# Kernel optimization log

Hardware: AMD Instinct MI355X
Metric: run time of the kernel (lower is better)

The kernel has to match this reference:

```python
import jax, jax.numpy as jnp
import numpy as np

Q_DIM = 2048
HEADS = 16
HEAD_DIM = 128
INNER = HEADS * HEAD_DIM          # 2048
MLP_HID = int(Q_DIM * 4.0)        # 8192
MLP_MULT = 2
EPS = 1e-05
B, S = 2, 2048


def setup_inputs() -> dict:
    key = jax.random.key(0)
    ks = jax.random.split(key, 4)
    hidden_states = jax.random.normal(ks[0], (B, S, Q_DIM), dtype=jnp.float32)
    # interleaved RoPE tables: cos/sin of shape [S, HEAD_DIM]
    half = HEAD_DIM // 2
    freqs = 1.0 / (10000.0 ** (np.arange(half, dtype=np.float64) / half))
    ang = np.outer(np.arange(S, dtype=np.float64), freqs)      # [S, half]
    ang = np.repeat(ang, 2, axis=-1)                            # [S, HEAD_DIM]
    rope_cos = jnp.asarray(np.cos(ang), dtype=jnp.float32)
    rope_sin = jnp.asarray(np.sin(ang), dtype=jnp.float32)
    fused_out = 3 * INNER + MLP_HID * MLP_MULT                  # 22528
    W_qkv_mlp = jax.random.normal(ks[1], (Q_DIM, fused_out), dtype=jnp.float32) * (Q_DIM ** -0.5)
    norm_q_w = jnp.ones((HEAD_DIM,), dtype=jnp.float32)
    norm_k_w = jnp.ones((HEAD_DIM,), dtype=jnp.float32)
    W_out = jax.random.normal(ks[2], (INNER + MLP_HID, Q_DIM), dtype=jnp.float32) * ((INNER + MLP_HID) ** -0.5)
    b_out = jnp.zeros((Q_DIM,), dtype=jnp.float32)
    return {"hidden_states": hidden_states, "rope_cos": rope_cos, "rope_sin": rope_sin,
            "W_qkv_mlp": W_qkv_mlp, "norm_q_w": norm_q_w, "norm_k_w": norm_k_w,
            "W_out": W_out, "b_out": b_out}


def _rms_norm(x, w):
    # RMSNorm over the last (head_dim) axis
    return x * jax.lax.rsqrt(jnp.mean(x * x, axis=-1, keepdims=True) + EPS) * w


def _apply_rope(x, cos, sin):
    # x: [B, S, H, D]; interleaved rotate-half (diffusers real-rope convention)
    xr = x.reshape(*x.shape[:-1], HEAD_DIM // 2, 2)
    rot = jnp.stack([-xr[..., 1], xr[..., 0]], axis=-1).reshape(x.shape)
    return x * cos[None, :, None, :] + rot * sin[None, :, None, :]


def reference(hidden_states, rope_cos, rope_sin, W_qkv_mlp, norm_q_w, norm_k_w, W_out, b_out):
    b, s, _ = hidden_states.shape
    proj = hidden_states @ W_qkv_mlp                              # [B,S,22528]
    qkv, mlp_h = jnp.split(proj, [3 * INNER], axis=-1)
    q, k, v = jnp.split(qkv, 3, axis=-1)
    q = q.reshape(b, s, HEADS, HEAD_DIM)
    k = k.reshape(b, s, HEADS, HEAD_DIM)
    v = v.reshape(b, s, HEADS, HEAD_DIM)
    q = _rms_norm(q, norm_q_w)
    k = _rms_norm(k, norm_k_w)
    q = _apply_rope(q, rope_cos, rope_sin)
    k = _apply_rope(k, rope_cos, rope_sin)
    scale = HEAD_DIM ** -0.5
    scores = jnp.einsum('bqhd,bkhd->bhqk', q, k) * scale          # [B,H,S,S]
    attn = jax.nn.softmax(scores, axis=-1)
    out_attn = jnp.einsum('bhqk,bkhd->bqhd', attn, v).reshape(b, s, INNER)
    m1, m2 = jnp.split(mlp_h, 2, axis=-1)                         # SwiGLU
    mlp_out = jax.nn.silu(m1) * m2                                # [B,S,MLP_HID]
    cat = jnp.concatenate([out_attn, mlp_out], axis=-1)           # [B,S,INNER+MLP_HID]
    return cat @ W_out + b_out
```

## Files before the change

### kernel.cpp

```cpp
#include <hip/hip_runtime.h>

typedef unsigned short u16;
typedef unsigned int u32;
typedef __bf16 bf16x8 __attribute__((ext_vector_type(8)));
typedef float f32x4 __attribute__((ext_vector_type(4)));

#define MFMA16(a, b, c) __builtin_amdgcn_mfma_f32_16x16x32_bf16((a), (b), (c), 0, 0, 0)

#define S_LEN 2048
#define D_HEAD 128
#define NHEADS 16
#define NBH 32
#define QDIM 2048
#define NPROJ 22528
#define NQKV 6144
#define NMLP 16384
#define NCAT 10240
#define MROWS 4096

#define BARRIER() __builtin_amdgcn_s_barrier()
#define WAITVM0() asm volatile("s_waitcnt vmcnt(0)" ::: "memory")

__device__ __forceinline__ float bf2f(u16 u) { return __uint_as_float(((u32)u) << 16); }
__device__ __forceinline__ u16 f2bf(float f) {
  u32 u = __float_as_uint(f);
  return (u16)((u + 0x7FFFu + ((u >> 16) & 1u)) >> 16);
}
__device__ __forceinline__ void gld16(const void* g, void* l) {
  __builtin_amdgcn_global_load_lds((__attribute__((address_space(1))) void*)(g),
                                   (__attribute__((address_space(3))) void*)(l), 16, 0, 0);
}

__global__ __launch_bounds__(256) void f32_to_bf16(const float* __restrict__ in,
                                                   u16* __restrict__ out) {
  const u32 i = blockIdx.x * 256 + threadIdx.x;
  const float4 v = ((const float4*)in)[i];
  uint2 o;
  o.x = (u32)f2bf(v.x) | ((u32)f2bf(v.y) << 16);
  o.y = (u32)f2bf(v.z) | ((u32)f2bf(v.w) << 16);
  ((uint2*)out)[i] = o;
}

template <int REMAP>
__global__ __launch_bounds__(256) void transpose_f32_bf16(const float* __restrict__ in,
                                                          u16* __restrict__ out, int R, int C) {
  __shared__ u16 tile[64][65];
  const int tx = threadIdx.x & 63;
  const int ty = threadIdx.x >> 6;
  const int c0 = blockIdx.x * 64;
  const int r0 = blockIdx.y * 64;
#pragma unroll
  for (int it = 0; it < 16; ++it) {
    const int rr = ty * 16 + it;
    tile[rr][tx] = f2bf(in[(size_t)(r0 + rr) * C + c0 + tx]);
  }
  __syncthreads();
#pragma unroll
  for (int it = 0; it < 16; ++it) {
    const int rr = ty * 16 + it;
    int orow = c0 + rr;
    if (REMAP && orow >= NQKV) {
      const int c = orow - NQKV;
      const int f = c & 8191;
      const int sel = c >> 13;
      orow = NQKV + (((f >> 4) << 5) | (sel << 4) | (f & 15));
    }
    out[(size_t)orow * R + r0 + tx] = tile[tx][rr];
  }
}

__global__ __launch_bounds__(256) void transpose_bf16_b(const u16* __restrict__ in,
                                                        u16* __restrict__ out, int R, int C) {
  __shared__ u16 tile[64][65];
  const int z = blockIdx.z;
  in += (size_t)z * R * C;
  out += (size_t)z * R * C;
  const int tx = threadIdx.x & 63;
  const int ty = threadIdx.x >> 6;
  const int c0 = blockIdx.x * 64;
  const int r0 = blockIdx.y * 64;
#pragma unroll
  for (int it = 0; it < 16; ++it) {
    const int rr = ty * 16 + it;
    tile[rr][tx] = in[(size_t)(r0 + rr) * C + c0 + tx];
  }
  __syncthreads();
#pragma unroll
  for (int it = 0; it < 16; ++it) {
    const int rr = ty * 16 + it;
    out[(size_t)(c0 + rr) * R + r0 + tx] = tile[tx][rr];
  }
}

template <int OUTMODE>
__global__ __launch_bounds__(256, 2) void gemm_bt(const u16* __restrict__ A,
                                                  const u16* __restrict__ Bt,
                                                  void* __restrict__ Cvoid,
                                                  const float* __restrict__ bias, int N, int K) {
  __shared__ u16 As[128 * 64];
  __shared__ u16 Bs[128 * 64];
  const int t = threadIdx.x;
  const int l = t & 63;
  const int w = t >> 6;
  const int lr = l & 15;
  const int lg = l >> 4;
  const int m0 = blockIdx.y * 128;
  const int n0 = blockIdx.x * 128;
  const int wm = (w >> 1) * 64;
  const int wn = (w & 1) * 64;

  f32x4 acc[4][4] = {};
  const int obase = w * 1024 + l * 16;

  for (int k0 = 0; k0 < K; k0 += 64) {
#pragma unroll
    for (int rnd = 0; rnd < 4; ++rnd) {
      const int o = obase + rnd * 4096;
      const int row = o >> 7;
      const int g = (o & 127) >> 4;
      const int gs = g ^ (row & 7);
      gld16(A + (size_t)(m0 + row) * K + k0 + gs * 8, &As[rnd * 2048 + w * 512]);
      gld16(Bt + (size_t)(n0 + row) * K + k0 + gs * 8, &Bs[rnd * 2048 + w * 512]);
    }
    __syncthreads();

    bf16x8 af[4][2], bfr[4][2];
#pragma unroll
    for (int i = 0; i < 4; ++i) {
#pragma unroll
      for (int kc = 0; kc < 2; ++kc) {
        const int ra = wm + i * 16 + lr;
        af[i][kc] = *(const bf16x8*)&As[ra * 64 + (((kc * 4 + lg) ^ (ra & 7)) * 8)];
        const int rb = wn + i * 16 + lr;
        bfr[i][kc] = *(const bf16x8*)&Bs[rb * 64 + (((kc * 4 + lg) ^ (rb & 7)) * 8)];
      }
    }
#pragma unroll
    for (int kc = 0; kc < 2; ++kc)
#pragma unroll
      for (int i = 0; i < 4; ++i)
#pragma unroll
        for (int j = 0; j < 4; ++j)
          acc[i][j] = MFMA16(af[i][kc], bfr[j][kc], acc[i][j]);
    __syncthreads();
  }

  if (OUTMODE == 1) {
    float* C = (float*)Cvoid;
#pragma unroll
    for (int i = 0; i < 4; ++i)
#pragma unroll
      for (int j = 0; j < 4; ++j)
#pragma unroll
        for (int r = 0; r < 4; ++r) {
          const int row = m0 + wm + i * 16 + lg * 4 + r;
          const int col = n0 + wn + j * 16 + lr;
          C[(size_t)row * N + col] = acc[i][j][r] + bias[col];
        }
  } else {
    u16* C = (u16*)Cvoid;
#pragma unroll
    for (int i = 0; i < 4; ++i)
#pragma unroll
      for (int jj = 0; jj < 2; ++jj)
#pragma unroll
        for (int r = 0; r < 4; ++r) {
          const int row = m0 + wm + i * 16 + lg * 4 + r;
          const float a1 = acc[i][2 * jj][r];
          const float a2 = acc[i][2 * jj + 1][r];
          const float fz = a1 / (1.f + __expf(-a1)) * a2;
          const int col = ((n0 + wn) >> 1) + jj * 16 + lr;
          C[(size_t)row * N + col] = f2bf(fz);
        }
  }
}

__global__ __launch_bounds__(256, 2) void gemm_qkv(const u16* __restrict__ A,
                                                   const u16* __restrict__ Bt,
                                                   const float* __restrict__ cosT,
                                                   const float* __restrict__ sinT,
                                                   const float* __restrict__ wq,
                                                   const float* __restrict__ wk,
                                                   u16* __restrict__ Qb, u16* __restrict__ Kb,
                                                   u16* __restrict__ Vb, int K) {
  __shared__ u16 As[128 * 64];
  __shared__ u16 Bs[128 * 64];
  __shared__ float redbuf[2][128];
  const int t = threadIdx.x;
  const int l = t & 63;
  const int w = t >> 6;
  const int lr = l & 15;
  const int lg = l >> 4;
  const int m0 = blockIdx.y * 128;
  const int n0 = blockIdx.x * 128;
  const int wm = (w >> 1) * 64;
  const int wn = (w & 1) * 64;

  f32x4 acc[4][4] = {};
  const int obase = w * 1024 + l * 16;

  for (int k0 = 0; k0 < K; k0 += 64) {
#pragma unroll
    for (int rnd = 0; rnd < 4; ++rnd) {
      const int o = obase + rnd * 4096;
      const int row = o >> 7;
      const int g = (o & 127) >> 4;
      const int gs = g ^ (row & 7);
      gld16(A + (size_t)(m0 + row) * K + k0 + gs * 8, &As[rnd * 2048 + w * 512]);
      gld16(Bt + (size_t)(n0 + row) * K + k0 + gs * 8, &Bs[rnd * 2048 + w * 512]);
    }
    __syncthreads();

    bf16x8 af[4][2], bfr[4][2];
#pragma unroll
    for (int i = 0; i < 4; ++i) {
#pragma unroll
      for (int kc = 0; kc < 2; ++kc) {
        const int ra = wm + i * 16 + lr;
        af[i][kc] = *(const bf16x8*)&As[ra * 64 + (((kc * 4 + lg) ^ (ra & 7)) * 8)];
        const int rb = wn + i * 16 + lr;
        bfr[i][kc] = *(const bf16x8*)&Bs[rb * 64 + (((kc * 4 + lg) ^ (rb & 7)) * 8)];
      }
    }
#pragma unroll
    for (int kc = 0; kc < 2; ++kc)
#pragma unroll
      for (int i = 0; i < 4; ++i)
#pragma unroll
        for (int j = 0; j < 4; ++j)
          acc[i][j] = MFMA16(af[i][kc], bfr[j][kc], acc[i][j]);
    __syncthreads();
  }

  const int type = n0 >> 11;
  const int h = (n0 >> 7) & 15;
  u16* dst = (type == 0) ? Qb : (type == 1) ? Kb : Vb;

  if (type == 2) {
#pragma unroll
    for (int i = 0; i < 4; ++i)
#pragma unroll
      for (int j = 0; j < 4; ++j)
#pragma unroll
        for (int r = 0; r < 4; ++r) {
          const int row = m0 + wm + i * 16 + lg * 4 + r;
          const int s = row & 2047, b = row >> 11;
          const int col = wn + j * 16 + lr;
          dst[((size_t)(b * 16 + h) * S_LEN + s) * 128 + col] = f2bf(acc[i][j][r]);
        }
    return;
  }

  float ssum[4][4];
#pragma unroll
  for (int i = 0; i < 4; ++i)
#pragma unroll
    for (int r = 0; r < 4; ++r) {
      float p = acc[i][0][r] * acc[i][0][r] + acc[i][1][r] * acc[i][1][r] +
                acc[i][2][r] * acc[i][2][r] + acc[i][3][r] * acc[i][3][r];
      p += __shfl_xor(p, 1);
      p += __shfl_xor(p, 2);
      p += __shfl_xor(p, 4);
      p += __shfl_xor(p, 8);
      ssum[i][r] = p;
    }
  if (lr == 0) {
#pragma unroll
    for (int i = 0; i < 4; ++i)
#pragma unroll
      for (int r = 0; r < 4; ++r) redbuf[wn >> 6][wm + i * 16 + lg * 4 + r] = ssum[i][r];
  }
  __syncthreads();

  const float* wgt = type ? wk : wq;
  const float sc = type ? 1.0f : 0.12751744f;
#pragma unroll
  for (int i = 0; i < 4; ++i)
#pragma unroll
    for (int r = 0; r < 4; ++r) {
      const int lrow = wm + i * 16 + lg * 4 + r;
      const float tot = redbuf[0][lrow] + redbuf[1][lrow];
      const float rsq = rsqrtf(tot * (1.0f / 128.0f) + 1e-5f) * sc;
      const int row = m0 + lrow;
      const int s = row & 2047, b = row >> 11;
      const size_t rbase = ((size_t)(b * 16 + h) * S_LEN + s) * 128;
#pragma unroll
      for (int j = 0; j < 4; ++j) {
        const int col = wn + j * 16 + lr;
        const float xn = acc[i][j][r] * rsq * wgt[col];
        const float pr = __shfl_xor(xn, 1);
        const float c = cosT[s * 128 + col];
        const float sn = sinT[s * 128 + col];
        const float val = (col & 1) ? (xn * c + pr * sn) : (xn * c - pr * sn);
        dst[rbase + col] = f2bf(val);
      }
    }
}

__global__ __launch_bounds__(256, 2) void attn_fwd(const u16* __restrict__ Qb,
                                                   const u16* __restrict__ Kb,
                                                   const u16* __restrict__ Vt,
                                                   u16* __restrict__ Cat) {
  __shared__ u16 Ks[2][64 * 128];
  __shared__ u16 Vs[2][128 * 64];
  __shared__ u16 Ps[4][32 * 64];

  const int t = threadIdx.x;
  const int l = t & 63;
  const int w = t >> 6;
  const int lr = l & 15;
  const int lg = l >> 4;
  const int swz = (blockIdx.x & 7) * 64 + (blockIdx.x >> 3);
  const int qt = swz & 15;
  const int bh = swz >> 4;
  const int b = bh >> 4;
  const int h = bh & 15;
  const int q0 = qt * 128 + w * 32;
  const int obase = w * 1024 + l * 16;

  const size_t kbase = (size_t)bh * S_LEN * 128;
  const size_t vbase = (size_t)bh * 128 * S_LEN;

  bf16x8 qf[2][4];
#pragma unroll
  for (int im = 0; im < 2; ++im)
#pragma unroll
    for (int kc = 0; kc < 4; ++kc)
      qf[im][kc] =
          *(const bf16x8*)&Qb[((size_t)bh * S_LEN + q0 + im * 16 + lr) * 128 + kc * 32 + lg * 8];

  f32x4 oacc[2][8] = {};
  float lrun[2][4] = {};

  u16* P = Ps[w];

  auto stageKV = [&](int buf, int kt2) {
    const int kk0 = kt2 * 64;
#pragma unroll
    for (int rnd = 0; rnd < 4; ++rnd) {
      const int o = obase + rnd * 4096;
      {
        const int key = o >> 8;
        const int g = (o & 255) >> 4;
        const int gs = g ^ (key & 7);
        gld16(Kb + kbase + (size_t)(kk0 + key) * 128 + gs * 8,
              &Ks[buf][rnd * 2048 + w * 512]);
      }
      {
        const int d = o >> 7;
        const int g = (o & 127) >> 4;
        const int gs = g ^ (d & 7);
        gld16(Vt + vbase + (size_t)d * S_LEN + kk0 + gs * 8,
              &Vs[buf][rnd * 2048 + w * 512]);
      }
    }
  };

  stageKV(0, 0);
  WAITVM0();
  BARRIER();

  int cur = 0;
  for (int kt = 0; kt < 32; ++kt) {
    if (kt + 1 < 32) stageKV(cur ^ 1, kt + 1);

    const u16* Kc = &Ks[cur][0];
    const u16* Vc = &Vs[cur][0];

    f32x4 sf[2][4] = {};
    __builtin_amdgcn_s_setprio(1);
#pragma unroll
    for (int j = 0; j < 4; ++j) {
      const int kr = j * 16 + lr;
      bf16x8 kf[4];
#pragma unroll
      for (int kc = 0; kc < 4; ++kc)
        kf[kc] = *(const bf16x8*)&Kc[kr * 128 + (((kc * 4 + lg) ^ (kr & 7)) * 8)];
#pragma unroll
      for (int kc = 0; kc < 4; ++kc)
#pragma unroll
        for (int im = 0; im < 2; ++im)
          sf[im][j] = MFMA16(qf[im][kc], kf[kc], sf[im][j]);
    }
    __builtin_amdgcn_s_setprio(0);

#pragma unroll
    for (int im = 0; im < 2; ++im)
#pragma unroll
      for (int r = 0; r < 4; ++r) {
        float psum = 0.f;
#pragma unroll
        for (int j = 0; j < 4; ++j) {
          const float pv = exp2f(sf[im][j][r]);
          sf[im][j][r] = pv;
          psum += pv;
        }
        lrun[im][r] += psum;
      }

#pragma unroll
    for (int im = 0; im < 2; ++im)
#pragma unroll
      for (int j = 0; j < 4; ++j)
#pragma unroll
        for (int r = 0; r < 4; ++r) {
          const int q = im * 16 + lg * 4 + r;
          const int key = j * 16 + lr;
          const int g = key >> 3;
          P[q * 64 + ((g ^ (q & 7)) * 8) + (key & 7)] = f2bf(sf[im][j][r]);
        }

    __builtin_amdgcn_s_setprio(1);
#pragma unroll
    for (int kc = 0; kc < 2; ++kc) {
      bf16x8 pa[2];
#pragma unroll
      for (int im = 0; im < 2; ++im) {
        const int q = im * 16 + lr;
        pa[im] = *(const bf16x8*)&P[q * 64 + (((kc * 4 + lg) ^ (q & 7)) * 8)];
      }
#pragma unroll
      for (int df = 0; df < 8; ++df) {
        const int d = df * 16 + lr;
        const bf16x8 vb = *(const bf16x8*)&Vc[d * 64 + (((kc * 4 + lg) ^ (d & 7)) * 8)];
#pragma unroll
        for (int im = 0; im < 2; ++im) oacc[im][df] = MFMA16(pa[im], vb, oacc[im][df]);
      }
    }
    __builtin_amdgcn_s_setprio(0);

    WAITVM0();
    BARRIER();
    cur ^= 1;
  }

#pragma unroll
  for (int im = 0; im < 2; ++im)
#pragma unroll
    for (int r = 0; r < 4; ++r) {
      float tot = lrun[im][r];
      tot += __shfl_xor(tot, 1);
      tot += __shfl_xor(tot, 2);
      tot += __shfl_xor(tot, 4);
      tot += __shfl_xor(tot, 8);
      const float inv = 1.0f / tot;
      const int row = b * S_LEN + q0 + im * 16 + lg * 4 + r;
#pragma unroll
      for (int df = 0; df < 8; ++df) {
        const int col = h * 128 + df * 16 + lr;
        Cat[(size_t)row * NCAT + col] = f2bf(oacc[im][df][r] * inv);
      }
    }
}

extern "C" void kernel_launch(void* const* d_in, const int* in_sizes, int n_in, void* d_out,
                              int out_size, void* d_ws, size_t ws_size, hipStream_t stream) {
  (void)in_sizes; (void)n_in; (void)out_size; (void)ws_size;
  const float* hs = (const float*)d_in[0];
  const float* rcos = (const float*)d_in[1];
  const float* rsin = (const float*)d_in[2];
  const float* Wqkv = (const float*)d_in[3];
  const float* wq = (const float*)d_in[4];
  const float* wk = (const float*)d_in[5];
  const float* Wout = (const float*)d_in[6];
  const float* bout = (const float*)d_in[7];
  float* out = (float*)d_out;

  char* ws = (char*)d_ws;
  size_t off = 0;
  auto nxt = [&](size_t bytes) {
    char* p = ws + off;
    off += (bytes + 255) & ~(size_t)255;
    return p;
  };
  u16* Xb = (u16*)nxt((size_t)MROWS * QDIM * 2);
  u16* Wqkvt = (u16*)nxt((size_t)NPROJ * QDIM * 2);
  u16* Woutt = (u16*)nxt((size_t)QDIM * NCAT * 2);
  u16* Qb = (u16*)nxt((size_t)NBH * S_LEN * D_HEAD * 2);
  u16* Kb = (u16*)nxt((size_t)NBH * S_LEN * D_HEAD * 2);
  u16* Vb = (u16*)nxt((size_t)NBH * S_LEN * D_HEAD * 2);
  u16* Vt = (u16*)nxt((size_t)NBH * S_LEN * D_HEAD * 2);
  u16* Cat = (u16*)nxt((size_t)MROWS * NCAT * 2);

  f32_to_bf16<<<(MROWS * QDIM / 4) / 256, 256, 0, stream>>>(hs, Xb);
  transpose_f32_bf16<1><<<dim3(NPROJ / 64, QDIM / 64), 256, 0, stream>>>(Wqkv, Wqkvt, QDIM,
                                                                         NPROJ);
  transpose_f32_bf16<0><<<dim3(QDIM / 64, NCAT / 64), 256, 0, stream>>>(Wout, Woutt, NCAT, QDIM);

  gemm_qkv<<<dim3(NQKV / 128, MROWS / 128), 256, 0, stream>>>(Xb, Wqkvt, rcos, rsin, wq, wk,
                                                              Qb, Kb, Vb, QDIM);
  gemm_bt<2><<<dim3(NMLP / 128, MROWS / 128), 256, 0, stream>>>(
      Xb, Wqkvt + (size_t)NQKV * QDIM, Cat + QDIM, nullptr, NCAT, QDIM);

  transpose_bf16_b<<<dim3(D_HEAD / 64, S_LEN / 64, NBH), 256, 0, stream>>>(Vb, Vt, S_LEN, D_HEAD);

  attn_fwd<<<S_LEN / 128 * NBH, 256, 0, stream>>>(Qb, Kb, Vt, Cat);

  gemm_bt<1><<<dim3(QDIM / 128, MROWS / 128), 256, 0, stream>>>(Cat, Woutt, out, bout, QDIM,
                                                                NCAT);
}
```

Measured before the change: 772.9 us.

## Fuse V transpose into QKV GEMM epilogue and widen weight transpose tiles

The QKV GEMM now writes V directly in transposed [bh][d][s] layout by staging the tile through swizzled shared memory, which removes the separate V transpose kernel and its intermediate buffer. The fp32-to-bf16 weight transpose now processes 64x256 tiles and writes 8-byte vectorized stores instead of scalar 2-byte stores, to improve write coalescing. The larger shared tile (64x260 u16) lowers occupancy for the transpose kernels, and the V epilogue adds an extra barrier and shared-memory round trip.

Measured after the change: 769.1 us. No clear change (-0.5%).

```diff
diff --git a/kernel.cpp b/kernel.cpp
--- a/kernel.cpp
+++ b/kernel.cpp
@@ -44,51 +44,37 @@
 template <int REMAP>
 __global__ __launch_bounds__(256) void transpose_f32_bf16(const float* __restrict__ in,
                                                           u16* __restrict__ out, int R, int C) {
-  __shared__ u16 tile[64][65];
-  const int tx = threadIdx.x & 63;
-  const int ty = threadIdx.x >> 6;
+  __shared__ u16 tile[64][260];
+  const int t = threadIdx.x;
+  const int tx = t & 63;
+  const int ty = t >> 6;
   const int c0 = blockIdx.x * 64;
-  const int r0 = blockIdx.y * 64;
-#pragma unroll
-  for (int it = 0; it < 16; ++it) {
-    const int rr = ty * 16 + it;
-    tile[rr][tx] = f2bf(in[(size_t)(r0 + rr) * C + c0 + tx]);
+  const int r0 = blockIdx.y * 256;
+
+#pragma unroll 8
+  for (int it = 0; it < 64; ++it) {
+    const int rr = it * 4 + ty;
+    tile[tx][rr] = f2bf(in[(size_t)(r0 + rr) * C + c0 + tx]);
   }
   __syncthreads();
-#pragma unroll
-  for (int it = 0; it < 16; ++it) {
-    const int rr = ty * 16 + it;
-    int orow = c0 + rr;
+
+  const int pos = t & 63;
+#pragma unroll 4
+  for (int i = 0; i < 16; ++i) {
+    const int cc = i * 4 + (t >> 6);
+    int orow = c0 + cc;
     if (REMAP && orow >= NQKV) {
       const int c = orow - NQKV;
       const int f = c & 8191;
       const int sel = c >> 13;
       orow = NQKV + (((f >> 4) << 5) | (sel << 4) | (f & 15));
     }
-    out[(size_t)orow * R + r0 + tx] = tile[tx][rr];
-  }
-}
-
-__global__ __launch_bounds__(256) void transpose_bf16_b(const u16* __restrict__ in,
-                                                        u16* __restrict__ out, int R, int C) {
-  __shared__ u16 tile[64][65];
-  const int z = blockIdx.z;
-  in += (size_t)z * R * C;
-  out += (size_t)z * R * C;
-  const int tx = threadIdx.x & 63;
-  const int ty = threadIdx.x >> 6;
-  const int c0 = blockIdx.x * 64;
-  const int r0 = blockIdx.y * 64;
-#pragma unroll
-  for (int it = 0; it < 16; ++it) {
-    const int rr = ty * 16 + it;
-    tile[rr][tx] = in[(size_t)(r0 + rr) * C + c0 + tx];
-  }
-  __syncthreads();
-#pragma unroll
-  for (int it = 0; it < 16; ++it) {
-    const int rr = ty * 16 + it;
-    out[(size_t)(c0 + rr) * R + r0 + tx] = tile[tx][rr];
+    const u32 lo = (u32)tile[cc][pos * 4] | ((u32)tile[cc][pos * 4 + 1] << 16);
+    const u32 hi = (u32)tile[cc][pos * 4 + 2] | ((u32)tile[cc][pos * 4 + 3] << 16);
+    uint2 v;
+    v.x = lo;
+    v.y = hi;
+    *(uint2*)&out[(size_t)orow * R + r0 + pos * 4] = v;
   }
 }
 
@@ -182,10 +168,11 @@
                                                    const float* __restrict__ wq,
                                                    const float* __restrict__ wk,
                                                    u16* __restrict__ Qb, u16* __restrict__ Kb,
-                                                   u16* __restrict__ Vb, int K) {
-  __shared__ u16 As[128 * 64];
-  __shared__ u16 Bs[128 * 64];
+                                                   u16* __restrict__ Vt, int K) {
+  __shared__ u16 smem[2][128 * 64];
   __shared__ float redbuf[2][128];
+  u16* As = smem[0];
+  u16* Bs = smem[1];
   const int t = threadIdx.x;
   const int l = t & 63;
   const int w = t >> 6;
@@ -206,8 +193,8 @@
       const int row = o >> 7;
       const int g = (o & 127) >> 4;
       const int gs = g ^ (row & 7);
-      gld16(A + (size_t)(m0 + row) * K + k0 + gs * 8, &As[rnd * 2048 + w * 512]);
-      gld16(Bt + (size_t)(n0 + row) * K + k0 + gs * 8, &Bs[rnd * 2048 + w * 512]);
+      gld16(A + (size_t)(m0 + row) * K + k0 + gs * 8, As + rnd * 2048 + w * 512);
+      gld16(Bt + (size_t)(n0 + row) * K + k0 + gs * 8, Bs + rnd * 2048 + w * 512);
     }
     __syncthreads();
 
@@ -234,22 +221,34 @@
 
   const int type = n0 >> 11;
   const int h = (n0 >> 7) & 15;
-  u16* dst = (type == 0) ? Qb : (type == 1) ? Kb : Vb;
+  const int b = m0 >> 11;
+  const int s0 = m0 & 2047;
+  const int bh = b * 16 + h;
 
   if (type == 2) {
+    u16* vt = smem[0];
 #pragma unroll
     for (int i = 0; i < 4; ++i)
 #pragma unroll
       for (int j = 0; j < 4; ++j)
 #pragma unroll
         for (int r = 0; r < 4; ++r) {
-          const int row = m0 + wm + i * 16 + lg * 4 + r;
-          const int s = row & 2047, b = row >> 11;
-          const int col = wn + j * 16 + lr;
-          dst[((size_t)(b * 16 + h) * S_LEN + s) * 128 + col] = f2bf(acc[i][j][r]);
+          const int s_loc = wm + i * 16 + lg * 4 + r;
+          const int d = wn + j * 16 + lr;
+          vt[d * 128 + (s_loc ^ ((d & 7) << 3))] = f2bf(acc[i][j][r]);
         }
+    __syncthreads();
+    const int g = t & 15;
+#pragma unroll
+    for (int i = 0; i < 8; ++i) {
+      const int d2 = i * 16 + (t >> 4);
+      const bf16x8 v = *(const bf16x8*)&vt[d2 * 128 + ((g ^ (d2 & 7)) * 8)];
+      *(bf16x8*)&Vt[((size_t)(bh * 128 + d2)) * S_LEN + s0 + g * 8] = v;
+    }
     return;
   }
+
+  u16* dst = (type == 0) ? Qb : Kb;
 
   float ssum[4][4];
 #pragma unroll
@@ -281,9 +280,8 @@
       const int lrow = wm + i * 16 + lg * 4 + r;
       const float tot = redbuf[0][lrow] + redbuf[1][lrow];
       const float rsq = rsqrtf(tot * (1.0f / 128.0f) + 1e-5f) * sc;
-      const int row = m0 + lrow;
-      const int s = row & 2047, b = row >> 11;
-      const size_t rbase = ((size_t)(b * 16 + h) * S_LEN + s) * 128;
+      const int s = (m0 + lrow) & 2047;
+      const size_t rbase = ((size_t)bh * S_LEN + s) * 128;
 #pragma unroll
       for (int j = 0; j < 4; ++j) {
         const int col = wn + j * 16 + lr;
@@ -478,22 +476,20 @@
   u16* Woutt = (u16*)nxt((size_t)QDIM * NCAT * 2);
   u16* Qb = (u16*)nxt((size_t)NBH * S_LEN * D_HEAD * 2);
   u16* Kb = (u16*)nxt((size_t)NBH * S_LEN * D_HEAD * 2);
-  u16* Vb = (u16*)nxt((size_t)NBH * S_LEN * D_HEAD * 2);
   u16* Vt = (u16*)nxt((size_t)NBH * S_LEN * D_HEAD * 2);
   u16* Cat = (u16*)nxt((size_t)MROWS * NCAT * 2);
 
   f32_to_bf16<<<(MROWS * QDIM / 4) / 256, 256, 0, stream>>>(hs, Xb);
-  transpose_f32_bf16<1><<<dim3(NPROJ / 64, QDIM / 64), 256, 0, stream>>>(Wqkv, Wqkvt, QDIM,
-                                                                         NPROJ);
-  transpose_f32_bf16<0><<<dim3(QDIM / 64, NCAT / 64), 256, 0, stream>>>(Wout, Woutt, NCAT, QDIM);
+  transpose_f32_bf16<1><<<dim3(NPROJ / 64, QDIM / 256), 256, 0, stream>>>(Wqkv, Wqkvt, QDIM,
+                                                                          NPROJ);
+  transpose_f32_bf16<0><<<dim3(QDIM / 64, NCAT / 256), 256, 0, stream>>>(Wout, Woutt, NCAT,
+                                                                         QDIM);
 
   gemm_qkv<<<dim3(NQKV / 128, MROWS / 128), 256, 0, stream>>>(Xb, Wqkvt, rcos, rsin, wq, wk,
-                                                              Qb, Kb, Vb, QDIM);
+                                                              Qb, Kb, Vt, QDIM);
   gemm_bt<2><<<dim3(NMLP / 128, MROWS / 128), 256, 0, stream>>>(
       Xb, Wqkvt + (size_t)NQKV * QDIM, Cat + QDIM, nullptr, NCAT, QDIM);
 
-  transpose_bf16_b<<<dim3(D_HEAD / 64, S_LEN / 64, NBH), 256, 0, stream>>>(Vb, Vt, S_LEN, D_HEAD);
-
   attn_fwd<<<S_LEN / 128 * NBH, 256, 0, stream>>>(Qb, Kb, Vt, Cat);
 
   gemm_bt<1><<<dim3(QDIM / 128, MROWS / 128), 256, 0, stream>>>(Cat, Woutt, out, bout, QDIM,
```
